# Performance work log

Measured on AMD Instinct MI355X. Metric: run time of the kernel, lower is better.

The kernel has to match this reference:

```python
import jax, jax.numpy as jnp
import numpy as np

N = 25000      # nodes
E = 200000     # edges (avg degree 8)
DIN = 512      # input_dim
HID = 512      # hidden_dim


def setup_inputs() -> dict:
    key = jax.random.key(0)
    ks = jax.random.split(key, 8)
    x = jax.random.normal(ks[0], (N, DIN), jnp.float32)
    edge_index = jax.random.randint(ks[1], (2, E), 0, N, jnp.int32)
    s_in = 1.0 / np.sqrt(DIN).astype(np.float32)
    s_h = 1.0 / np.sqrt(HID).astype(np.float32)
    W1 = jax.random.normal(ks[2], (DIN, HID), jnp.float32) * s_in
    b1 = jnp.zeros((HID,), jnp.float32)
    W2 = jax.random.normal(ks[3], (HID, HID), jnp.float32) * s_h
    b2 = jnp.zeros((HID,), jnp.float32)
    Wo = jax.random.normal(ks[4], (HID, 1), jnp.float32) * s_h
    bo = jnp.zeros((1,), jnp.float32)
    Ww = jax.random.normal(ks[5], (HID, 1), jnp.float32) * s_h
    bw = jnp.zeros((1,), jnp.float32)
    return dict(x=x, edge_index=edge_index, W1=W1, b1=b1, W2=W2, b2=b2,
                Wo=Wo, bo=bo, Ww=Ww, bw=bw)


def reference(x, edge_index, W1, b1, W2, b2, Wo, bo, Ww, bw):
    n = x.shape[0]
    src, dst = edge_index[0], edge_index[1]
    # GCNConv with self-loops: deg counts incoming edges + 1 self-loop
    deg = jax.ops.segment_sum(jnp.ones(src.shape[0], x.dtype), dst,
                              num_segments=n) + 1.0
    dis = jax.lax.rsqrt(deg)              # deg^{-1/2}, [N]
    norm = dis[src] * dis[dst]            # per-edge symmetric norm, [E]

    def gcn(h, W, b):
        hw = h @ W                        # [N, H] dense GEMM
        msg = hw[src] * norm[:, None]     # gather + scale, [E, H]
        agg = jax.ops.segment_sum(msg, dst, num_segments=n)
        agg = agg + hw * (dis * dis)[:, None]  # self-loop contribution
        return agg + b

    h1 = jax.nn.relu(gcn(x, W1, b1))
    h2 = jax.nn.relu(gcn(h1, W2, b2))
    open_logits = (h2 @ Wo + bo)[:, 0]
    wall_logits = (h2 @ Ww + bw)[:, 0]
    return open_logits, wall_logits
```

## Files before the change

### kernel.cpp

```cpp
#include <hip/hip_runtime.h>
#include <hip/hip_bf16.h>

#define DIN 512
#define HID 512

#define AS1 __attribute__((address_space(1)))
#define AS3 __attribute__((address_space(3)))

typedef __attribute__((ext_vector_type(8))) short bfrag;
typedef __attribute__((ext_vector_type(4))) float ffrag;
typedef __attribute__((ext_vector_type(8))) unsigned short u16x8;
typedef __attribute__((ext_vector_type(4))) unsigned short u16x4;

__global__ __launch_bounds__(256) void prelude(const float* __restrict__ x,
                                               unsigned short* __restrict__ xb,
                                               const float* __restrict__ W1,
                                               const float* __restrict__ W2,
                                               unsigned short* __restrict__ Wt1,
                                               unsigned short* __restrict__ Wt2,
                                               const int* __restrict__ dst,
                                               int* __restrict__ cnt,
                                               int E, int Nvalid, int C1) {
    int b = blockIdx.x;
    if (b < C1) {
        int idx = b * 256 + threadIdx.x;
        int row = idx >> 6;
        int c = (idx & 63) * 8;
        unsigned short o[8];
        if (row < Nvalid) {
            float4 a = *(const float4*)&x[(size_t)row * 512 + c];
            float4 v = *(const float4*)&x[(size_t)row * 512 + c + 4];
            __hip_bfloat16 t;
            t = __float2bfloat16(a.x); o[0] = *(unsigned short*)&t;
            t = __float2bfloat16(a.y); o[1] = *(unsigned short*)&t;
            t = __float2bfloat16(a.z); o[2] = *(unsigned short*)&t;
            t = __float2bfloat16(a.w); o[3] = *(unsigned short*)&t;
            t = __float2bfloat16(v.x); o[4] = *(unsigned short*)&t;
            t = __float2bfloat16(v.y); o[5] = *(unsigned short*)&t;
            t = __float2bfloat16(v.z); o[6] = *(unsigned short*)&t;
            t = __float2bfloat16(v.w); o[7] = *(unsigned short*)&t;
        } else {
#pragma unroll
            for (int j = 0; j < 8; ++j) o[j] = 0;
        }
        *(u16x8*)&xb[(size_t)row * 512 + c] = *(u16x8*)o;
    } else if (b < C1 + 512) {
        int bb = b - C1;
        int which = bb >> 8;
        bb &= 255;
        const float* W = which ? W2 : W1;
        unsigned short* Wt = which ? Wt2 : Wt1;
        __shared__ float t[32][33];
        int tid = threadIdx.x;
        int tx = tid & 31, ty = tid >> 5;
        int n0 = (bb & 15) * 32, k0 = (bb >> 4) * 32;
#pragma unroll
        for (int s = 0; s < 4; ++s)
            t[ty + 8 * s][tx] = W[(size_t)(k0 + ty + 8 * s) * 512 + n0 + tx];
        __syncthreads();
#pragma unroll
        for (int s = 0; s < 4; ++s) {
            __hip_bfloat16 v = __float2bfloat16(t[tx][ty + 8 * s]);
            Wt[(size_t)(n0 + ty + 8 * s) * 512 + k0 + tx] = *(unsigned short*)&v;
        }
    } else {
        int e = (b - C1 - 512) * 256 + threadIdx.x;
        if (e < E) atomicAdd(&cnt[dst[e]], 1);
    }
}

__global__ __launch_bounds__(256) void scanA(const int* __restrict__ cnt, int* __restrict__ tmp,
                                             int* __restrict__ bsum, int N) {
    int tid = threadIdx.x, lane = tid & 63, wave = tid >> 6;
    int i = blockIdx.x * 256 + tid;
    int v = (i < N) ? cnt[i] : 0;
    int incl = v;
#pragma unroll
    for (int o = 1; o < 64; o <<= 1) {
        int t = __shfl_up(incl, o);
        if (lane >= o) incl += t;
    }
    __shared__ int wtot[4];
    if (lane == 63) wtot[wave] = incl;
    __syncthreads();
    int woff = 0;
#pragma unroll
    for (int w = 0; w < 4; ++w) woff += (w < wave) ? wtot[w] : 0;
    if (i < N) tmp[i] = woff + incl - v;
    if (tid == 255) bsum[blockIdx.x] = woff + incl;
}

__global__ __launch_bounds__(256) void scanB(const int* __restrict__ cnt,
                                             const int* __restrict__ tmp,
                                             const int* __restrict__ bsum,
                                             int* __restrict__ offs,
                                             int* __restrict__ cursor,
                                             float* __restrict__ dis,
                                             float* __restrict__ out,
                                             const float* __restrict__ bo,
                                             const float* __restrict__ bw,
                                             int N, int nb) {
    int tid = threadIdx.x;
    int lane = tid & 63, wv = tid >> 6;
    int v  = (tid < nb) ? bsum[tid] : 0;
    int vb = (tid < (int)blockIdx.x) ? v : 0;
    int a = v, bfr = vb;
#pragma unroll
    for (int o = 32; o > 0; o >>= 1) {
        a   += __shfl_down(a, o);
        bfr += __shfl_down(bfr, o);
    }
    __shared__ int sa[4], sb[4];
    if (lane == 0) { sa[wv] = a; sb[wv] = bfr; }
    __syncthreads();
    int totalE = sa[0] + sa[1] + sa[2] + sa[3];
    int before = sb[0] + sb[1] + sb[2] + sb[3];

    int i = blockIdx.x * 256 + tid;
    if (i < N) {
        int o = tmp[i] + before;
        offs[i] = o;
        cursor[i] = o;
        int d = cnt[i];
        dis[i] = rsqrtf((float)d + 1.0f);
        out[i] = bo[0];
        out[N + i] = bw[0];
    }
    if (blockIdx.x == 0 && tid == 0) offs[N] = totalE;
}

__device__ inline bool tile_map2(int b, int Mtiles, int& m0, int& n0) {
    int xcd = b & 7, i = b >> 3;
    int nt = i & 1, mg = i >> 1;
    int mt = mg * 8 + xcd;
    if (mt >= Mtiles) return false;
    m0 = mt * 128;
    n0 = nt * 256;
    return true;
}

__device__ __forceinline__ void gemm_body(const short* __restrict__ A,
                                          const short* __restrict__ B,
                                          unsigned short* __restrict__ C,
                                          int Mtiles, int bidx,
                                          short* As, short* Bs) {
    const int K = 512;
    int m0, n0;
    if (!tile_map2(bidx, Mtiles, m0, n0)) return;
    int tid = threadIdx.x;
    int lane = tid & 63, wave = tid >> 6;
    int wm = (wave & 1) * 64;
    int wn = (wave >> 1) * 128;
    int r = lane & 15, q = lane >> 4;

    unsigned aoff[4]; int aldso[4];
#pragma unroll
    for (int i = 0; i < 4; ++i) {
        int s = i * 256 + tid;
        int row = s >> 3;
        int c = (s & 7) ^ (row & 7);
        aoff[i] = (unsigned)(m0 + row) * K + c * 8;
        aldso[i] = (i * 256 + (tid & ~63)) * 8;
    }
    unsigned boff[8]; int bldso[8];
#pragma unroll
    for (int i = 0; i < 8; ++i) {
        int s = i * 256 + tid;
        int row = s >> 3;
        int c = (s & 7) ^ (row & 7);
        boff[i] = (unsigned)(n0 + row) * K + c * 8;
        bldso[i] = (i * 256 + (tid & ~63)) * 8;
    }

    ffrag acc[4][8];
#pragma unroll
    for (int i = 0; i < 4; ++i)
#pragma unroll
        for (int j = 0; j < 8; ++j) acc[i][j] = ffrag{0.f, 0.f, 0.f, 0.f};

    for (int k0 = 0; k0 < K; k0 += 64) {
#pragma unroll
        for (int i = 0; i < 4; ++i)
            __builtin_amdgcn_global_load_lds((const AS1 void*)(A + aoff[i] + k0),
                                             (AS3 void*)(As + aldso[i]), 16, 0, 0);
#pragma unroll
        for (int i = 0; i < 8; ++i)
            __builtin_amdgcn_global_load_lds((const AS1 void*)(B + boff[i] + k0),
                                             (AS3 void*)(Bs + bldso[i]), 16, 0, 0);
        __syncthreads();

#pragma unroll
        for (int s2 = 0; s2 < 2; ++s2) {
            bfrag af[4], bfr[8];
#pragma unroll
            for (int i = 0; i < 4; ++i) {
                int arow = wm + i * 16 + r;
                int ach = (s2 * 4 + q) ^ (arow & 7);
                af[i] = *(const bfrag*)&As[arow * 64 + ach * 8];
            }
#pragma unroll
            for (int j = 0; j < 8; ++j) {
                int brow = wn + j * 16 + r;
                int bch = (s2 * 4 + q) ^ (brow & 7);
                bfr[j] = *(const bfrag*)&Bs[brow * 64 + bch * 8];
            }
#pragma unroll
            for (int i = 0; i < 4; ++i)
#pragma unroll
                for (int j = 0; j < 8; ++j)
                    acc[i][j] = __builtin_amdgcn_mfma_f32_16x16x32_bf16(bfr[j], af[i], acc[i][j], 0, 0, 0);
        }
        __syncthreads();
    }

#pragma unroll
    for (int i = 0; i < 4; ++i) {
        int m = m0 + wm + i * 16 + r;
#pragma unroll
        for (int j = 0; j < 8; ++j) {
            int n = n0 + wn + j * 16 + q * 4;
            u16x4 o;
#pragma unroll
            for (int reg = 0; reg < 4; ++reg) {
                __hip_bfloat16 v = __float2bfloat16(acc[i][j][reg]);
                o[reg] = *(unsigned short*)&v;
            }
            *(u16x4*)&C[(size_t)m * 512 + n] = o;
        }
    }
}

__global__ __launch_bounds__(256, 2) void gemm_fill(const short* __restrict__ A,
                                                    const short* __restrict__ B,
                                                    unsigned short* __restrict__ C,
                                                    int Mtiles, int G,
                                                    const int* __restrict__ src,
                                                    const int* __restrict__ dst,
                                                    int* __restrict__ cursor,
                                                    const float* __restrict__ dis,
                                                    int2* __restrict__ csr2, int E) {
    __shared__ __align__(16) short As[128 * 64];
    __shared__ __align__(16) short Bs[256 * 64];
    int b = blockIdx.x;
    if (b < G) {
        gemm_body(A, B, C, Mtiles, b, As, Bs);
    } else {
        int e = (b - G) * 256 + threadIdx.x;
        if (e >= E) return;
        int d = dst[e];
        int s = src[e];
        int pos = atomicAdd(&cursor[d], 1);
        int2 rec;
        rec.x = s << 10;
        rec.y = __float_as_int(dis[s] * dis[d]);
        csr2[pos] = rec;
    }
}

__global__ __launch_bounds__(256, 2) void gemm_bf16(const short* __restrict__ A,
                                                    const short* __restrict__ B,
                                                    unsigned short* __restrict__ C,
                                                    int Mtiles) {
    __shared__ __align__(16) short As[128 * 64];
    __shared__ __align__(16) short Bs[256 * 64];
    gemm_body(A, B, C, Mtiles, blockIdx.x, As, Bs);
}

__device__ inline void cvt8(u16x8 v, float* f) {
#pragma unroll
    for (int j = 0; j < 8; ++j) f[j] = __uint_as_float((unsigned)v[j] << 16);
}

__global__ __launch_bounds__(256) void agg_relu_sh(const unsigned short* __restrict__ hw,
                                                   const int2* __restrict__ csr2,
                                                   const int* __restrict__ offs,
                                                   const float* __restrict__ dis,
                                                   const float* __restrict__ bias,
                                                   unsigned short* __restrict__ out,
                                                   int N, int Mpad) {
    int b = blockIdx.x;
    int shard = b & 7;
    int tid = threadIdx.x;
    int wave = tid >> 6, lane = tid & 63;
    int cluster = lane >> 3;
    int sub = lane & 7;
    int node = (b >> 3) * 32 + wave * 8 + cluster;
    int c0 = shard * 64 + sub * 8;
    if (node >= N) {
        if (node < Mpad) {
            u16x8 z = {0, 0, 0, 0, 0, 0, 0, 0};
            *(u16x8*)&out[(size_t)node * HID + c0] = z;
        }
        return;
    }

    const char* hwb = (const char*)hw + c0 * 2;
    float dn = dis[node];
    int e0 = offs[node], e1 = offs[node + 1];

    float acc[8];
    {
        u16x8 sv = *(const u16x8*)&hw[(size_t)node * HID + c0];
        float g[8];
        cvt8(sv, g);
        float4 bb0 = *(const float4*)&bias[c0];
        float4 bb1 = *(const float4*)&bias[c0 + 4];
        float dis2 = dn * dn;
        acc[0] = g[0] * dis2 + bb0.x; acc[1] = g[1] * dis2 + bb0.y;
        acc[2] = g[2] * dis2 + bb0.z; acc[3] = g[3] * dis2 + bb0.w;
        acc[4] = g[4] * dis2 + bb1.x; acc[5] = g[5] * dis2 + bb1.y;
        acc[6] = g[6] * dis2 + bb1.z; acc[7] = g[7] * dis2 + bb1.w;
    }

    for (int e = e0; e < e1; e += 4) {
        int off[4]; float wgt[4];
#pragma unroll
        for (int t = 0; t < 4; ++t) {
            int ee = e + t;
            int ec = (ee < e1) ? ee : (e1 - 1);
            int2 rec = csr2[ec];
            off[t] = rec.x;
            wgt[t] = (ee < e1) ? __int_as_float(rec.y) : 0.f;
        }
        u16x8 v[4];
#pragma unroll
        for (int t = 0; t < 4; ++t)
            v[t] = *(const u16x8*)(hwb + off[t]);
#pragma unroll
        for (int t = 0; t < 4; ++t) {
            float g[8];
            cvt8(v[t], g);
#pragma unroll
            for (int u = 0; u < 8; ++u) acc[u] += g[u] * wgt[t];
        }
    }

    unsigned short o[8];
#pragma unroll
    for (int t = 0; t < 8; ++t) {
        __hip_bfloat16 v = __float2bfloat16(fmaxf(acc[t], 0.f));
        o[t] = *(unsigned short*)&v;
    }
    *(u16x8*)&out[(size_t)node * HID + c0] = *(u16x8*)o;
}

__global__ __launch_bounds__(256) void agg_heads_sh(const unsigned short* __restrict__ hw,
                                                    const int2* __restrict__ csr2,
                                                    const int* __restrict__ offs,
                                                    const float* __restrict__ dis,
                                                    const float* __restrict__ bias,
                                                    const float* __restrict__ Wo,
                                                    const float* __restrict__ Ww,
                                                    float* __restrict__ out, int N) {
    int b = blockIdx.x;
    int shard = b & 7;
    int tid = threadIdx.x;
    int wave = tid >> 6, lane = tid & 63;
    int cluster = lane >> 3;
    int sub = lane & 7;
    int node = (b >> 3) * 32 + wave * 8 + cluster;
    if (node >= N) return;
    int c0 = shard * 64 + sub * 8;

    const char* hwb = (const char*)hw + c0 * 2;
    float dn = dis[node];
    int e0 = offs[node], e1 = offs[node + 1];

    float acc[8];
    {
        u16x8 sv = *(const u16x8*)&hw[(size_t)node * HID + c0];
        float g[8];
        cvt8(sv, g);
        float4 bb0 = *(const float4*)&bias[c0];
        float4 bb1 = *(const float4*)&bias[c0 + 4];
        float dis2 = dn * dn;
        acc[0] = g[0] * dis2 + bb0.x; acc[1] = g[1] * dis2 + bb0.y;
        acc[2] = g[2] * dis2 + bb0.z; acc[3] = g[3] * dis2 + bb0.w;
        acc[4] = g[4] * dis2 + bb1.x; acc[5] = g[5] * dis2 + bb1.y;
        acc[6] = g[6] * dis2 + bb1.z; acc[7] = g[7] * dis2 + bb1.w;
    }

    for (int e = e0; e < e1; e += 4) {
        int off[4]; float wgt[4];
#pragma unroll
        for (int t = 0; t < 4; ++t) {
            int ee = e + t;
            int ec = (ee < e1) ? ee : (e1 - 1);
            int2 rec = csr2[ec];
            off[t] = rec.x;
            wgt[t] = (ee < e1) ? __int_as_float(rec.y) : 0.f;
        }
        u16x8 v[4];
#pragma unroll
        for (int t = 0; t < 4; ++t)
            v[t] = *(const u16x8*)(hwb + off[t]);
#pragma unroll
        for (int t = 0; t < 4; ++t) {
            float g[8];
            cvt8(v[t], g);
#pragma unroll
            for (int u = 0; u < 8; ++u) acc[u] += g[u] * wgt[t];
        }
    }

    float4 wo0 = *(const float4*)&Wo[c0];
    float4 wo1 = *(const float4*)&Wo[c0 + 4];
    float4 ww0 = *(const float4*)&Ww[c0];
    float4 ww1 = *(const float4*)&Ww[c0 + 4];
    float po = 0.f, pw = 0.f, h;
    h = fmaxf(acc[0], 0.f); po += h * wo0.x; pw += h * ww0.x;
    h = fmaxf(acc[1], 0.f); po += h * wo0.y; pw += h * ww0.y;
    h = fmaxf(acc[2], 0.f); po += h * wo0.z; pw += h * ww0.z;
    h = fmaxf(acc[3], 0.f); po += h * wo0.w; pw += h * ww0.w;
    h = fmaxf(acc[4], 0.f); po += h * wo1.x; pw += h * ww1.x;
    h = fmaxf(acc[5], 0.f); po += h * wo1.y; pw += h * ww1.y;
    h = fmaxf(acc[6], 0.f); po += h * wo1.z; pw += h * ww1.z;
    h = fmaxf(acc[7], 0.f); po += h * wo1.w; pw += h * ww1.w;

#pragma unroll
    for (int off2 = 4; off2 > 0; off2 >>= 1) {
        po += __shfl_down(po, off2);
        pw += __shfl_down(pw, off2);
    }
    if (sub == 0) {
        atomicAdd(&out[node], po);
        atomicAdd(&out[N + node], pw);
    }
}

extern "C" void kernel_launch(void* const* d_in, const int* in_sizes, int n_in,
                              void* d_out, int out_size, void* d_ws, size_t ws_size,
                              hipStream_t stream) {
    const float* x  = (const float*)d_in[0];
    const int*   ei = (const int*)d_in[1];
    const float* W1 = (const float*)d_in[2];
    const float* b1 = (const float*)d_in[3];
    const float* W2 = (const float*)d_in[4];
    const float* b2 = (const float*)d_in[5];
    const float* Wo = (const float*)d_in[6];
    const float* bo = (const float*)d_in[7];
    const float* Ww = (const float*)d_in[8];
    const float* bw = (const float*)d_in[9];

    const int N = in_sizes[0] / DIN;
    const int E = in_sizes[1] / 2;
    const int Mpad = (N + 127) & ~127;
    const int Mtiles = Mpad / 128;
    const int nb = (N + 255) / 256;
    const int C1 = Mpad / 4;
    const int EJ = (E + 255) / 256;

    char* ws = (char*)d_ws;
    size_t p = 0;
    auto alloc = [&](size_t bytes) -> char* {
        char* r = ws + p;
        p += (bytes + 255) & ~(size_t)255;
        return r;
    };
    int*   cnt    = (int*)alloc((size_t)N * 4);
    int*   offs   = (int*)alloc((size_t)(N + 1) * 4);
    int*   cursor = (int*)alloc((size_t)N * 4);
    int*   tmp    = (int*)alloc((size_t)N * 4);
    int*   bsum   = (int*)alloc(132 * 4);
    float* dis    = (float*)alloc((size_t)N * 4);
    int2*  csr2   = (int2*)alloc((size_t)E * 8 + 64);
    unsigned short* xb  = (unsigned short*)alloc((size_t)Mpad * 512 * 2);
    unsigned short* Wt1 = (unsigned short*)alloc((size_t)512 * 512 * 2);
    unsigned short* Wt2 = (unsigned short*)alloc((size_t)512 * 512 * 2);
    unsigned short* hw  = (unsigned short*)alloc((size_t)Mpad * 512 * 2);
    unsigned short* h1  = (unsigned short*)alloc((size_t)Mpad * 512 * 2);

    const int* src = ei;
    const int* dst = ei + E;

    hipMemsetAsync(cnt, 0, (size_t)N * 4, stream);

    prelude<<<C1 + 512 + EJ, 256, 0, stream>>>(x, xb, W1, W2, Wt1, Wt2,
                                               dst, cnt, E, N, C1);
    scanA<<<nb, 256, 0, stream>>>(cnt, tmp, bsum, N);
    scanB<<<nb, 256, 0, stream>>>(cnt, tmp, bsum, offs, cursor, dis,
                                  (float*)d_out, bo, bw, N, nb);

    const int G = 8 * ((Mtiles + 7) / 8) * 2;
    gemm_fill<<<G + EJ, 256, 0, stream>>>((const short*)xb, (const short*)Wt1, hw,
                                          Mtiles, G, src, dst, cursor, dis, csr2, E);
    agg_relu_sh<<<8 * (Mpad / 32), 256, 0, stream>>>(hw, csr2, offs, dis, b1, h1, N, Mpad);
    gemm_bf16<<<G, 256, 0, stream>>>((const short*)h1, (const short*)Wt2, hw, Mtiles);
    agg_heads_sh<<<8 * ((N + 31) / 32), 256, 0, stream>>>(hw, csr2, offs, dis, b2,
                                                          Wo, Ww, (float*)d_out, N);
}
```

Measured before the change: 224.5 us.

## Switch GEMM to 256x256 tiles with double-buffered LDS prefetch pipeline

Both bf16 GEMMs now use 256x256 output tiles computed by 512-thread workgroups, replacing 128x256 tiles on 256 threads. The LDS is double-buffered: the next K-slab is issued through global_load_lds while the current one feeds the MFMAs, with an explicit vmcnt wait and s_setprio around the MFMA bursts. A new XCD-aware tile mapping spreads contiguous tiles across XCDs, and the edge-fill tail now runs 512 edges per block. This should hide global load latency and raise operand reuse per tile. The cost is fewer workgroups than CUs (about 196) and 128KB of LDS per block, which limits occupancy to one block per CU.

```diff
diff --git a/kernel.cpp b/kernel.cpp
--- a/kernel.cpp
+++ b/kernel.cpp
@@ -11,6 +11,8 @@
 typedef __attribute__((ext_vector_type(4))) float ffrag;
 typedef __attribute__((ext_vector_type(8))) unsigned short u16x8;
 typedef __attribute__((ext_vector_type(4))) unsigned short u16x4;
+
+#define WAIT_VMCNT(n) asm volatile("s_waitcnt vmcnt(" #n ")" ::: "memory")
 
 __global__ __launch_bounds__(256) void prelude(const float* __restrict__ x,
                                                unsigned short* __restrict__ xb,
@@ -129,95 +131,116 @@
     if (blockIdx.x == 0 && tid == 0) offs[N] = totalE;
 }
 
-__device__ inline bool tile_map2(int b, int Mtiles, int& m0, int& n0) {
+__device__ inline bool tile_map256(int b, int nwg, int& m0, int& n0) {
+    if (b >= nwg) return false;
+    int q = nwg >> 3, rr = nwg & 7;
     int xcd = b & 7, i = b >> 3;
-    int nt = i & 1, mg = i >> 1;
-    int mt = mg * 8 + xcd;
-    if (mt >= Mtiles) return false;
-    m0 = mt * 128;
+    int wgid = (xcd < rr ? xcd * (q + 1) : rr * (q + 1) + (xcd - rr) * q) + i;
+    int mt = wgid >> 1, nt = wgid & 1;
+    m0 = mt * 256;
     n0 = nt * 256;
     return true;
 }
 
-__device__ __forceinline__ void gemm_body(const short* __restrict__ A,
-                                          const short* __restrict__ B,
-                                          unsigned short* __restrict__ C,
-                                          int Mtiles, int bidx,
-                                          short* As, short* Bs) {
-    const int K = 512;
+__device__ __forceinline__ void gemm_body256(const short* __restrict__ A,
+                                             const short* __restrict__ B,
+                                             unsigned short* __restrict__ C,
+                                             int nwg, int bidx, short* lds) {
     int m0, n0;
-    if (!tile_map2(bidx, Mtiles, m0, n0)) return;
+    if (!tile_map256(bidx, nwg, m0, n0)) return;
     int tid = threadIdx.x;
     int lane = tid & 63, wave = tid >> 6;
-    int wm = (wave & 1) * 64;
-    int wn = (wave >> 1) * 128;
+    int wm = (wave >> 2) * 128;
+    int wn = (wave & 3) * 64;
     int r = lane & 15, q = lane >> 4;
 
-    unsigned aoff[4]; int aldso[4];
+    unsigned aoff[4], boff[4];
+    int ldso[4];
 #pragma unroll
     for (int i = 0; i < 4; ++i) {
-        int s = i * 256 + tid;
+        int s = i * 512 + tid;
         int row = s >> 3;
         int c = (s & 7) ^ (row & 7);
-        aoff[i] = (unsigned)(m0 + row) * K + c * 8;
-        aldso[i] = (i * 256 + (tid & ~63)) * 8;
-    }
-    unsigned boff[8]; int bldso[8];
-#pragma unroll
-    for (int i = 0; i < 8; ++i) {
-        int s = i * 256 + tid;
-        int row = s >> 3;
-        int c = (s & 7) ^ (row & 7);
-        boff[i] = (unsigned)(n0 + row) * K + c * 8;
-        bldso[i] = (i * 256 + (tid & ~63)) * 8;
-    }
-
-    ffrag acc[4][8];
-#pragma unroll
-    for (int i = 0; i < 4; ++i)
-#pragma unroll
-        for (int j = 0; j < 8; ++j) acc[i][j] = ffrag{0.f, 0.f, 0.f, 0.f};
-
-    for (int k0 = 0; k0 < K; k0 += 64) {
+        aoff[i] = (unsigned)(m0 + row) * 512 + c * 8;
+        boff[i] = (unsigned)(n0 + row) * 512 + c * 8;
+        ldso[i] = (i * 512 + (tid & ~63)) * 8;
+    }
+
+    ffrag acc[8][4];
+#pragma unroll
+    for (int i = 0; i < 8; ++i)
+#pragma unroll
+        for (int j = 0; j < 4; ++j) acc[i][j] = ffrag{0.f, 0.f, 0.f, 0.f};
+
+    auto stageK = [&](int k0, int which) {
+        short* AsB = lds + which * 32768;
+        short* BsB = AsB + 16384;
 #pragma unroll
         for (int i = 0; i < 4; ++i)
             __builtin_amdgcn_global_load_lds((const AS1 void*)(A + aoff[i] + k0),
-                                             (AS3 void*)(As + aldso[i]), 16, 0, 0);
-#pragma unroll
-        for (int i = 0; i < 8; ++i)
+                                             (AS3 void*)(AsB + ldso[i]), 16, 0, 0);
+#pragma unroll
+        for (int i = 0; i < 4; ++i)
             __builtin_amdgcn_global_load_lds((const AS1 void*)(B + boff[i] + k0),
-                                             (AS3 void*)(Bs + bldso[i]), 16, 0, 0);
-        __syncthreads();
-
-#pragma unroll
-        for (int s2 = 0; s2 < 2; ++s2) {
-            bfrag af[4], bfr[8];
-#pragma unroll
-            for (int i = 0; i < 4; ++i) {
-                int arow = wm + i * 16 + r;
-                int ach = (s2 * 4 + q) ^ (arow & 7);
-                af[i] = *(const bfrag*)&As[arow * 64 + ach * 8];
-            }
-#pragma unroll
-            for (int j = 0; j < 8; ++j) {
+                                             (AS3 void*)(BsB + ldso[i]), 16, 0, 0);
+    };
+
+    auto computeK = [&](int which) {
+        const short* As = lds + which * 32768;
+        const short* Bs = As + 16384;
+#pragma unroll
+        for (int qk = 0; qk < 2; ++qk) {
+            bfrag bfr[4];
+#pragma unroll
+            for (int j = 0; j < 4; ++j) {
                 int brow = wn + j * 16 + r;
-                int bch = (s2 * 4 + q) ^ (brow & 7);
+                int bch = (qk * 4 + q) ^ (brow & 7);
                 bfr[j] = *(const bfrag*)&Bs[brow * 64 + bch * 8];
             }
 #pragma unroll
-            for (int i = 0; i < 4; ++i)
-#pragma unroll
-                for (int j = 0; j < 8; ++j)
-                    acc[i][j] = __builtin_amdgcn_mfma_f32_16x16x32_bf16(bfr[j], af[i], acc[i][j], 0, 0, 0);
-        }
-        __syncthreads();
-    }
-
-#pragma unroll
-    for (int i = 0; i < 4; ++i) {
-        int m = m0 + wm + i * 16 + r;
-#pragma unroll
-        for (int j = 0; j < 8; ++j) {
+            for (int qm = 0; qm < 2; ++qm) {
+                bfrag af[4];
+#pragma unroll
+                for (int i2 = 0; i2 < 4; ++i2) {
+                    int arow = wm + qm * 64 + i2 * 16 + r;
+                    int ach = (qk * 4 + q) ^ (arow & 7);
+                    af[i2] = *(const bfrag*)&As[arow * 64 + ach * 8];
+                }
+                __builtin_amdgcn_s_setprio(1);
+#pragma unroll
+                for (int i2 = 0; i2 < 4; ++i2)
+#pragma unroll
+                    for (int j = 0; j < 4; ++j)
+                        acc[qm * 4 + i2][j] = __builtin_amdgcn_mfma_f32_16x16x32_bf16(
+                            bfr[j], af[i2], acc[qm * 4 + i2][j], 0, 0, 0);
+                __builtin_amdgcn_s_setprio(0);
+            }
+        }
+    };
+
+    stageK(0, 0);
+    int cur = 0;
+#pragma unroll 1
+    for (int kt = 0; kt < 7; ++kt) {
+        stageK((kt + 1) * 64, cur ^ 1);
+        WAIT_VMCNT(8);
+        __builtin_amdgcn_s_barrier();
+        __builtin_amdgcn_sched_barrier(0);
+        computeK(cur);
+        __builtin_amdgcn_sched_barrier(0);
+        __builtin_amdgcn_s_barrier();
+        cur ^= 1;
+    }
+    WAIT_VMCNT(0);
+    __builtin_amdgcn_s_barrier();
+    __builtin_amdgcn_sched_barrier(0);
+    computeK(cur);
+
+#pragma unroll
+    for (int i = 0; i < 8; ++i) {
+        int m = m0 + wm + (i >> 2) * 64 + (i & 3) * 16 + r;
+#pragma unroll
+        for (int j = 0; j < 4; ++j) {
             int n = n0 + wn + j * 16 + q * 4;
             u16x4 o;
 #pragma unroll
@@ -230,22 +253,21 @@
     }
 }
 
-__global__ __launch_bounds__(256, 2) void gemm_fill(const short* __restrict__ A,
+__global__ __launch_bounds__(512, 2) void gemm_fill(const short* __restrict__ A,
                                                     const short* __restrict__ B,
                                                     unsigned short* __restrict__ C,
-                                                    int Mtiles, int G,
+                                                    int nwg, int G,
                                                     const int* __restrict__ src,
                                                     const int* __restrict__ dst,
                                                     int* __restrict__ cursor,
                                                     const float* __restrict__ dis,
                                                     int2* __restrict__ csr2, int E) {
-    __shared__ __align__(16) short As[128 * 64];
-    __shared__ __align__(16) short Bs[256 * 64];
+    __shared__ __align__(16) short lds[65536];
     int b = blockIdx.x;
     if (b < G) {
-        gemm_body(A, B, C, Mtiles, b, As, Bs);
+        gemm_body256(A, B, C, nwg, b, lds);
     } else {
-        int e = (b - G) * 256 + threadIdx.x;
+        int e = (b - G) * 512 + threadIdx.x;
         if (e >= E) return;
         int d = dst[e];
         int s = src[e];
@@ -257,13 +279,12 @@
     }
 }
 
-__global__ __launch_bounds__(256, 2) void gemm_bf16(const short* __restrict__ A,
+__global__ __launch_bounds__(512, 2) void gemm_bf16(const short* __restrict__ A,
                                                     const short* __restrict__ B,
                                                     unsigned short* __restrict__ C,
-                                                    int Mtiles) {
-    __shared__ __align__(16) short As[128 * 64];
-    __shared__ __align__(16) short Bs[256 * 64];
-    gemm_body(A, B, C, Mtiles, blockIdx.x, As, Bs);
+                                                    int nwg) {
+    __shared__ __align__(16) short lds[65536];
+    gemm_body256(A, B, C, nwg, blockIdx.x, lds);
 }
 
 __device__ inline void cvt8(u16x8 v, float* f) {
@@ -444,11 +465,12 @@
 
     const int N = in_sizes[0] / DIN;
     const int E = in_sizes[1] / 2;
-    const int Mpad = (N + 127) & ~127;
-    const int Mtiles = Mpad / 128;
+    const int Mpad = ((N + 255) / 256) * 256;
+    const int nwg = (Mpad / 256) * 2;
     const int nb = (N + 255) / 256;
     const int C1 = Mpad / 4;
     const int EJ = (E + 255) / 256;
+    const int EJ2 = (E + 511) / 512;
 
     char* ws = (char*)d_ws;
     size_t p = 0;
@@ -481,11 +503,10 @@
     scanB<<<nb, 256, 0, stream>>>(cnt, tmp, bsum, offs, cursor, dis,
                                   (float*)d_out, bo, bw, N, nb);
 
-    const int G = 8 * ((Mtiles + 7) / 8) * 2;
-    gemm_fill<<<G + EJ, 256, 0, stream>>>((const short*)xb, (const short*)Wt1, hw,
-                                          Mtiles, G, src, dst, cursor, dis, csr2, E);
+    gemm_fill<<<nwg + EJ2, 512, 0, stream>>>((const short*)xb, (const short*)Wt1, hw,
+                                             nwg, nwg, src, dst, cursor, dis, csr2, E);
     agg_relu_sh<<<8 * (Mpad / 32), 256, 0, stream>>>(hw, csr2, offs, dis, b1, h1, N, Mpad);
-    gemm_bf16<<<G, 256, 0, stream>>>((const short*)h1, (const short*)Wt2, hw, Mtiles);
+    gemm_bf16<<<nwg, 512, 0, stream>>>((const short*)h1, (const short*)Wt2, hw, nwg);
     agg_heads_sh<<<8 * ((N + 31) / 32), 256, 0, stream>>>(hw, csr2, offs, dis, b2,
                                                           Wo, Ww, (float*)d_out, N);
 }
```

New measurement: 230.7 us. 1.03x slower.

## Store GEMM outputs with per-row rotated column shards to spread gather traffic

Applied to the files above, without the earlier changes.

Each 64-column shard of the hw and h1 matrices is now stored at a position rotated by the row index. GEMM epilogues write in this rotated layout, the aggregation kernels read and write through the matching rotation, and layer-2's GEMM un-rotates its A operand on load. The goal is to spread concurrent shard-sliced gathers across memory channels and banks instead of having all blocks for one shard hit the same address offsets. It adds index arithmetic and couples the layout across three kernels, which raises the risk of a mismatch.

```diff
diff --git a/kernel.cpp b/kernel.cpp
--- a/kernel.cpp
+++ b/kernel.cpp
@@ -11,6 +11,7 @@
 typedef __attribute__((ext_vector_type(4))) float ffrag;
 typedef __attribute__((ext_vector_type(8))) unsigned short u16x8;
 typedef __attribute__((ext_vector_type(4))) unsigned short u16x4;
+
 
 __global__ __launch_bounds__(256) void prelude(const float* __restrict__ x,
                                                unsigned short* __restrict__ xb,
@@ -139,6 +140,7 @@
     return true;
 }
 
+template <bool ROTA>
 __device__ __forceinline__ void gemm_body(const short* __restrict__ A,
                                           const short* __restrict__ B,
                                           unsigned short* __restrict__ C,
@@ -153,12 +155,13 @@
     int wn = (wave >> 1) * 128;
     int r = lane & 15, q = lane >> 4;
 
-    unsigned aoff[4]; int aldso[4];
+    unsigned aoff[4]; int aldso[4]; int arow_[4];
 #pragma unroll
     for (int i = 0; i < 4; ++i) {
         int s = i * 256 + tid;
         int row = s >> 3;
         int c = (s & 7) ^ (row & 7);
+        arow_[i] = m0 + row;
         aoff[i] = (unsigned)(m0 + row) * K + c * 8;
         aldso[i] = (i * 256 + (tid & ~63)) * 8;
     }
@@ -180,9 +183,13 @@
 
     for (int k0 = 0; k0 < K; k0 += 64) {
 #pragma unroll
-        for (int i = 0; i < 4; ++i)
-            __builtin_amdgcn_global_load_lds((const AS1 void*)(A + aoff[i] + k0),
+        for (int i = 0; i < 4; ++i) {
+            unsigned ka;
+            if (ROTA) ka = ((unsigned)(((k0 >> 6) + arow_[i]) & 7)) << 6;
+            else ka = (unsigned)k0;
+            __builtin_amdgcn_global_load_lds((const AS1 void*)(A + aoff[i] + ka),
                                              (AS3 void*)(As + aldso[i]), 16, 0, 0);
+        }
 #pragma unroll
         for (int i = 0; i < 8; ++i)
             __builtin_amdgcn_global_load_lds((const AS1 void*)(B + boff[i] + k0),
@@ -219,13 +226,14 @@
 #pragma unroll
         for (int j = 0; j < 8; ++j) {
             int n = n0 + wn + j * 16 + q * 4;
+            int np = ((((n >> 6) + m) & 7) << 6) | (n & 63);
             u16x4 o;
 #pragma unroll
             for (int reg = 0; reg < 4; ++reg) {
                 __hip_bfloat16 v = __float2bfloat16(acc[i][j][reg]);
                 o[reg] = *(unsigned short*)&v;
             }
-            *(u16x4*)&C[(size_t)m * 512 + n] = o;
+            *(u16x4*)&C[(size_t)m * 512 + np] = o;
         }
     }
 }
@@ -243,7 +251,7 @@
     __shared__ __align__(16) short Bs[256 * 64];
     int b = blockIdx.x;
     if (b < G) {
-        gemm_body(A, B, C, Mtiles, b, As, Bs);
+        gemm_body<false>(A, B, C, Mtiles, b, As, Bs);
     } else {
         int e = (b - G) * 256 + threadIdx.x;
         if (e >= E) return;
@@ -263,7 +271,7 @@
                                                     int Mtiles) {
     __shared__ __align__(16) short As[128 * 64];
     __shared__ __align__(16) short Bs[256 * 64];
-    gemm_body(A, B, C, Mtiles, blockIdx.x, As, Bs);
+    gemm_body<true>(A, B, C, Mtiles, blockIdx.x, As, Bs);
 }
 
 __device__ inline void cvt8(u16x8 v, float* f) {
@@ -286,21 +294,22 @@
     int sub = lane & 7;
     int node = (b >> 3) * 32 + wave * 8 + cluster;
     int c0 = shard * 64 + sub * 8;
+    int sgn = (shard + node) & 7;
     if (node >= N) {
         if (node < Mpad) {
             u16x8 z = {0, 0, 0, 0, 0, 0, 0, 0};
-            *(u16x8*)&out[(size_t)node * HID + c0] = z;
+            *(u16x8*)&out[(size_t)node * HID + sgn * 64 + sub * 8] = z;
         }
         return;
     }
 
-    const char* hwb = (const char*)hw + c0 * 2;
+    const char* hwb = (const char*)hw + sub * 16;
     float dn = dis[node];
     int e0 = offs[node], e1 = offs[node + 1];
 
     float acc[8];
     {
-        u16x8 sv = *(const u16x8*)&hw[(size_t)node * HID + c0];
+        u16x8 sv = *(const u16x8*)(hwb + ((size_t)node << 10) + sgn * 128);
         float g[8];
         cvt8(sv, g);
         float4 bb0 = *(const float4*)&bias[c0];
@@ -319,7 +328,8 @@
             int ee = e + t;
             int ec = (ee < e1) ? ee : (e1 - 1);
             int2 rec = csr2[ec];
-            off[t] = rec.x;
+            int sg = (((unsigned)rec.x >> 10) + shard) & 7;
+            off[t] = rec.x + sg * 128;
             wgt[t] = (ee < e1) ? __int_as_float(rec.y) : 0.f;
         }
         u16x8 v[4];
@@ -341,7 +351,7 @@
         __hip_bfloat16 v = __float2bfloat16(fmaxf(acc[t], 0.f));
         o[t] = *(unsigned short*)&v;
     }
-    *(u16x8*)&out[(size_t)node * HID + c0] = *(u16x8*)o;
+    *(u16x8*)&out[(size_t)node * HID + sgn * 64 + sub * 8] = *(u16x8*)o;
 }
 
 __global__ __launch_bounds__(256) void agg_heads_sh(const unsigned short* __restrict__ hw,
@@ -361,14 +371,15 @@
     int node = (b >> 3) * 32 + wave * 8 + cluster;
     if (node >= N) return;
     int c0 = shard * 64 + sub * 8;
-
-    const char* hwb = (const char*)hw + c0 * 2;
+    int sgn = (shard + node) & 7;
+
+    const char* hwb = (const char*)hw + sub * 16;
     float dn = dis[node];
     int e0 = offs[node], e1 = offs[node + 1];
 
     float acc[8];
     {
-        u16x8 sv = *(const u16x8*)&hw[(size_t)node * HID + c0];
+        u16x8 sv = *(const u16x8*)(hwb + ((size_t)node << 10) + sgn * 128);
         float g[8];
         cvt8(sv, g);
         float4 bb0 = *(const float4*)&bias[c0];
@@ -387,7 +398,8 @@
             int ee = e + t;
             int ec = (ee < e1) ? ee : (e1 - 1);
             int2 rec = csr2[ec];
-            off[t] = rec.x;
+            int sg = (((unsigned)rec.x >> 10) + shard) & 7;
+            off[t] = rec.x + sg * 128;
             wgt[t] = (ee < e1) ? __int_as_float(rec.y) : 0.f;
         }
         u16x8 v[4];
```

Result: no change. 222.5 us (-0.9%).
